# Kernel tuning notes

Hardware: AMD Instinct MI355X
Metric: run time of the kernel (lower is better)

## Reference

```python
import jax, jax.numpy as jnp
import numpy as np

NUM_V, NUM_R, ARITY = 100000, 1000, 3
D, I, H = 128, 64, 128
B, N = 4096, 64


def setup_inputs() -> dict:
    key = jax.random.key(0)
    ks = jax.random.split(key, 11)
    return {
        "r": jax.random.randint(ks[0], (B, N), 0, NUM_R),
        "e": jax.random.randint(ks[1], (ARITY, B, N), 0, NUM_V),
        "V": jax.random.normal(ks[2], (NUM_V, D + I), dtype=jnp.float32),
        "R": jax.random.normal(ks[3], (NUM_R, D), dtype=jnp.float32),
        "P": jax.random.normal(ks[4], (ARITY, D), dtype=jnp.float32),
        "WV": jax.random.normal(ks[5], (D + I, H), dtype=jnp.float32) * (1.0 / np.sqrt(D + I)),
        "bV": jax.random.normal(ks[6], (H,), dtype=jnp.float32) * 0.01,
        "WR": jax.random.normal(ks[7], (D, H), dtype=jnp.float32) * (1.0 / np.sqrt(D)),
        "bR": jax.random.normal(ks[8], (H,), dtype=jnp.float32) * 0.01,
        "WP": jax.random.normal(ks[9], (D, H), dtype=jnp.float32) * (1.0 / np.sqrt(D)),
        "bP": jax.random.normal(ks[10], (H,), dtype=jnp.float32) * 0.01,
    }


def reference(r, e, V, R, P, WV, bV, WR, bR, WP, bP):
    # x = Rl(R[r]) : gather relation embeddings then project -> [B, N, H]
    x = jnp.einsum("bnd,dh->bnh", R[r], WR) + bR
    # Pl(P[i]) for all arity positions at once -> [A, H]
    pe = P @ WP + bP
    # Vl(V[e[i]]) for all positions: gather then project -> [A, B, N, H]
    ve = jnp.einsum("abnd,dh->abnh", V[e], WV) + bV
    # loop body x = x * Pl(P[i]) * Vl(V[e[i]]) == product over arity axis
    x = x * jnp.prod(pe[:, None, None, :] * ve, axis=0)
    # dropout is identity (p=0 / eval); reduce over neighbor axis
    return jnp.sum(x, axis=1)  # [B, H]
```

## Files before the change

### kernel.cpp

```cpp
#include <hip/hip_runtime.h>

#define NUM_V 100000
#define NUM_R 1000
#define ARITY 3
#define DD 128
#define DI 192
#define HH 128
#define BB 4096
#define NN 64

typedef __attribute__((ext_vector_type(4))) float f32x4;
typedef __attribute__((ext_vector_type(8))) _Float16 half8;
typedef __attribute__((ext_vector_type(2))) _Float16 half2v;

__device__ inline void gload16(const void* g, void* lds) {
    __builtin_amdgcn_global_load_lds(
        (const __attribute__((address_space(1))) unsigned int*)g,
        (__attribute__((address_space(3))) unsigned int*)lds, 16, 0, 0);
}

__global__ __launch_bounds__(256) void prep_kernel(
    const float* __restrict__ R, const float* __restrict__ WR, const float* __restrict__ bR,
    _Float16* __restrict__ RWh,
    const float* __restrict__ WV, unsigned short* __restrict__ wf,
    const float* __restrict__ P, const float* __restrict__ WP, const float* __restrict__ bP,
    float* __restrict__ peProd) {
    const int bid = blockIdx.x;
    const int tid = threadIdx.x;

    if (bid < 32) {
        const int lane = tid & 63;
        const int wave = tid >> 6;
        const int wavesPerGrid = 32 * 4;
        const int waveId = bid * 4 + wave;
        const float2 b2 = ((const float2*)bR)[lane];
        const float2* __restrict__ W2 = (const float2*)WR;
        for (int rowBase0 = waveId * 8; rowBase0 < NUM_R; rowBase0 += wavesPerGrid * 8) {
            const int rowBase = __builtin_amdgcn_readfirstlane(rowBase0);
            float2 acc[8];
#pragma unroll
            for (int r8 = 0; r8 < 8; ++r8) acc[r8] = make_float2(0.f, 0.f);
#pragma unroll 4
            for (int k4 = 0; k4 < DD / 4; ++k4) {
                float4 v[8];
#pragma unroll
                for (int r8 = 0; r8 < 8; ++r8)
                    v[r8] = ((const float4*)(R + (size_t)(rowBase + r8) * DD))[k4];
#pragma unroll
                for (int kk = 0; kk < 4; ++kk) {
                    float2 w = W2[(k4 * 4 + kk) * 64 + lane];
#pragma unroll
                    for (int r8 = 0; r8 < 8; ++r8) {
                        float vv = (kk == 0) ? v[r8].x : (kk == 1) ? v[r8].y : (kk == 2) ? v[r8].z : v[r8].w;
                        acc[r8].x += vv * w.x;
                        acc[r8].y += vv * w.y;
                    }
                }
            }
#pragma unroll
            for (int r8 = 0; r8 < 8; ++r8) {
                if (rowBase + r8 < NUM_R) {
                    half2v h;
                    h.x = (_Float16)(acc[r8].x + b2.x);
                    h.y = (_Float16)(acc[r8].y + b2.y);
                    *(half2v*)(RWh + (size_t)(rowBase + r8) * HH + lane * 2) = h;
                }
            }
        }
    } else if (bid < 80) {
        if (tid < 64) {
            const int wb = bid - 32;
            const int ks = wb >> 3;
            const int ct = wb & 7;
            const int l = tid;
            const int col = ct * 16 + (l & 15);
            const int k0 = ks * 32 + (l >> 4) * 8;
            size_t base = (size_t)(ks * 8 + ct) * 512;
#pragma unroll
            for (int j = 0; j < 8; ++j) {
                float v = WV[(size_t)(k0 + j) * HH + col];
                wf[base + l * 8 + j] = __builtin_bit_cast(unsigned short, (_Float16)v);
            }
        }
    } else {
        if (tid < HH) {
            int h = tid;
            float prod = 1.0f;
            for (int a = 0; a < ARITY; ++a) {
                float acc = bP[h];
                for (int d = 0; d < DD; ++d) acc += P[a * DD + d] * WP[d * HH + h];
                prod *= acc;
            }
            peProd[h] = prod;
        }
    }
}

__global__ __launch_bounds__(832) void gemm_bres(const float* __restrict__ A,
                                                 const unsigned short* __restrict__ wf,
                                                 const float* __restrict__ bias,
                                                 _Float16* __restrict__ C, int M) {
    __shared__ unsigned short bsm[24576];
    __shared__ float aslots[13][2][1024];

    const int tid = threadIdx.x;
    const int l = tid & 63;
    const int wv = tid >> 6;

    const int tile = wv * 256 + blockIdx.x;
    const int rowbase = tile * 32;
    const bool active = rowbase < M;

    float bcol[8];
#pragma unroll
    for (int ct = 0; ct < 8; ++ct) bcol[ct] = bias[ct * 16 + (l & 15)];

    const float* aSrc = A + (size_t)(rowbase + (l >> 3)) * DI + (((l & 7) ^ (l >> 3)) << 2);

    int aoff[2][2];
#pragma unroll
    for (int rt = 0; rt < 2; ++rt) {
        const int Rr = rt * 16 + (l & 15);
        const int q = l >> 4;
#pragma unroll
        for (int k = 0; k < 2; ++k)
            aoff[rt][k] = Rr * 32 + (((2 * q + k) ^ (Rr & 7)) << 2);
    }

    f32x4 acc[2][8];
#pragma unroll
    for (int rt = 0; rt < 2; ++rt)
#pragma unroll
        for (int ct = 0; ct < 8; ++ct) acc[rt][ct] = (f32x4){0.f, 0.f, 0.f, 0.f};

#define STAGE_A(slot, ks)                                                   \
    do {                                                                    \
        _Pragma("unroll") for (int i = 0; i < 4; ++i)                       \
            gload16(aSrc + (ks) * 32 + i * 8 * DI, &aslots[wv][slot][i * 256]); \
    } while (0)

#define WAITV(n) asm volatile("s_waitcnt vmcnt(" #n ")" ::: "memory")

    if (active) {
        STAGE_A(0, 0);
        STAGE_A(1, 1);
    }
    if (wv < 12) {
#pragma unroll
        for (int i = 0; i < 4; ++i) {
            const int off = wv * 4096 + i * 1024;
            gload16((const char*)wf + off + l * 16, (char*)bsm + off);
        }
    }

    __syncthreads();
    if (!active) return;

#pragma unroll
    for (int ks = 0; ks < 6; ++ks) {
        const int slot = ks & 1;

        if (ks == 2 || ks == 3 || ks == 4) {
            WAITV(4);
            __builtin_amdgcn_sched_barrier(0);
        } else if (ks == 5) {
            WAITV(0);
            __builtin_amdgcn_sched_barrier(0);
        }

        f32x4 av[2][2];
#pragma unroll
        for (int rt = 0; rt < 2; ++rt) {
            av[rt][0] = *(const f32x4*)&aslots[wv][slot][aoff[rt][0]];
            av[rt][1] = *(const f32x4*)&aslots[wv][slot][aoff[rt][1]];
        }
        half8 bh[8];
#pragma unroll
        for (int ct = 0; ct < 8; ++ct)
            bh[ct] = *(const half8*)&bsm[(ks * 8 + ct) * 512 + l * 8];

        asm volatile("s_waitcnt lgkmcnt(0)" ::: "memory");
        __builtin_amdgcn_sched_barrier(0);

        if (ks < 4) STAGE_A(slot, ks + 2);

        half8 ah[2];
#pragma unroll
        for (int rt = 0; rt < 2; ++rt) {
            half8 t;
            t[0] = (_Float16)av[rt][0].x;
            t[1] = (_Float16)av[rt][0].y;
            t[2] = (_Float16)av[rt][0].z;
            t[3] = (_Float16)av[rt][0].w;
            t[4] = (_Float16)av[rt][1].x;
            t[5] = (_Float16)av[rt][1].y;
            t[6] = (_Float16)av[rt][1].z;
            t[7] = (_Float16)av[rt][1].w;
            ah[rt] = t;
        }

#pragma unroll
        for (int ct = 0; ct < 8; ++ct) {
#pragma unroll
            for (int rt = 0; rt < 2; ++rt)
                acc[rt][ct] = __builtin_amdgcn_mfma_f32_16x16x32_f16(ah[rt], bh[ct], acc[rt][ct], 0, 0, 0);
        }
    }
#undef STAGE_A
#undef WAITV

#pragma unroll
    for (int rt = 0; rt < 2; ++rt) {
        const int rb = rowbase + rt * 16 + (l >> 4) * 4;
#pragma unroll
        for (int j = 0; j < 4; ++j) {
            const int row = rb + j;
            if (row < M) {
#pragma unroll
                for (int ct = 0; ct < 8; ++ct)
                    C[(size_t)row * HH + ct * 16 + (l & 15)] = (_Float16)(acc[rt][ct][j] + bcol[ct]);
            }
        }
    }
}

__global__ __launch_bounds__(256) void gather_kernel(const int* __restrict__ r,
                                                     const int* __restrict__ e,
                                                     const _Float16* __restrict__ VWh,
                                                     const _Float16* __restrict__ RWh,
                                                     const float* __restrict__ peProd,
                                                     float* __restrict__ out) {
    __shared__ int rIdx[NN];
    __shared__ int eIdx[ARITY][NN];
    __shared__ float4 partial[3][16][2];

    const int b = blockIdx.x;
    const int tid = threadIdx.x;

    if (tid < NN) {
        rIdx[tid] = r[b * NN + tid];
    } else {
        int t = tid - NN;
        eIdx[t >> 6][t & 63] = e[(size_t)(t >> 6) * BB * NN + b * NN + (t & 63)];
    }
    __syncthreads();

    const int lane = tid & 63;
    const int wv = tid >> 6;
    const int q = lane >> 4;
    const int ho = lane & 15;

    float acc8[8];
#pragma unroll
    for (int k = 0; k < 8; ++k) acc8[k] = 0.f;

#pragma unroll
    for (int it = 0; it < 4; ++it) {
        int n = it * 16 + wv * 4 + q;
        half8 rw = *(const half8*)(RWh + (size_t)rIdx[n] * HH + ho * 8);
        half8 v0 = *(const half8*)(VWh + (size_t)eIdx[0][n] * HH + ho * 8);
        half8 v1 = *(const half8*)(VWh + (size_t)eIdx[1][n] * HH + ho * 8);
        half8 v2 = *(const half8*)(VWh + (size_t)eIdx[2][n] * HH + ho * 8);
        half8 p = rw * v0;
        p = p * v1;
        p = p * v2;
#pragma unroll
        for (int k = 0; k < 8; ++k) acc8[k] += (float)p[k];
    }

#pragma unroll
    for (int k = 0; k < 8; ++k) {
        acc8[k] += __shfl_xor(acc8[k], 16);
        acc8[k] += __shfl_xor(acc8[k], 32);
    }

    if (wv > 0 && lane < 16) {
        partial[wv - 1][ho][0] = make_float4(acc8[0], acc8[1], acc8[2], acc8[3]);
        partial[wv - 1][ho][1] = make_float4(acc8[4], acc8[5], acc8[6], acc8[7]);
    }
    __syncthreads();
    if (wv == 0 && lane < 16) {
        float4 s0 = make_float4(acc8[0], acc8[1], acc8[2], acc8[3]);
        float4 s1 = make_float4(acc8[4], acc8[5], acc8[6], acc8[7]);
#pragma unroll
        for (int g = 0; g < 3; ++g) {
            float4 t0 = partial[g][ho][0], t1 = partial[g][ho][1];
            s0.x += t0.x; s0.y += t0.y; s0.z += t0.z; s0.w += t0.w;
            s1.x += t1.x; s1.y += t1.y; s1.z += t1.z; s1.w += t1.w;
        }
        float4 p0 = ((const float4*)peProd)[ho * 2];
        float4 p1 = ((const float4*)peProd)[ho * 2 + 1];
        ((float4*)(out + (size_t)b * HH))[ho * 2] =
            make_float4(s0.x * p0.x, s0.y * p0.y, s0.z * p0.z, s0.w * p0.w);
        ((float4*)(out + (size_t)b * HH))[ho * 2 + 1] =
            make_float4(s1.x * p1.x, s1.y * p1.y, s1.z * p1.z, s1.w * p1.w);
    }
}

extern "C" void kernel_launch(void* const* d_in, const int* in_sizes, int n_in,
                              void* d_out, int out_size, void* d_ws, size_t ws_size,
                              hipStream_t stream) {
    const int* r = (const int*)d_in[0];
    const int* e = (const int*)d_in[1];
    const float* V = (const float*)d_in[2];
    const float* R = (const float*)d_in[3];
    const float* P = (const float*)d_in[4];
    const float* WV = (const float*)d_in[5];
    const float* bV = (const float*)d_in[6];
    const float* WR = (const float*)d_in[7];
    const float* bR = (const float*)d_in[8];
    const float* WP = (const float*)d_in[9];
    const float* bP = (const float*)d_in[10];
    float* out = (float*)d_out;

    _Float16* VWh = (_Float16*)d_ws;
    _Float16* RWh = VWh + (size_t)NUM_V * HH;
    float* peProd = (float*)(RWh + (size_t)NUM_R * HH);
    unsigned short* wfrag = (unsigned short*)(peProd + HH);

    prep_kernel<<<81, 256, 0, stream>>>(R, WR, bR, RWh, WV, wfrag, P, WP, bP, peProd);
    gemm_bres<<<256, 832, 0, stream>>>(V, wfrag, bV, VWh, NUM_V);
    gather_kernel<<<BB, 256, 0, stream>>>(r, e, VWh, RWh, peProd, out);
}
```

Measured before the change: 70.46 us.

## Replace 13-wave GEMM with 6-wave persistent multi-tile kernel loading B from global

Measured after the change: 87.78 us. +24.6%, slower.

```diff
diff --git a/kernel.cpp b/kernel.cpp
--- a/kernel.cpp
+++ b/kernel.cpp
@@ -96,129 +96,118 @@
     }
 }
 
-__global__ __launch_bounds__(832) void gemm_bres(const float* __restrict__ A,
-                                                 const unsigned short* __restrict__ wf,
-                                                 const float* __restrict__ bias,
-                                                 _Float16* __restrict__ C, int M) {
-    __shared__ unsigned short bsm[24576];
-    __shared__ float aslots[13][2][1024];
+__global__ __launch_bounds__(384) void gemm_dense(const float* __restrict__ A,
+                                                  const unsigned short* __restrict__ wf,
+                                                  const float* __restrict__ bias,
+                                                  _Float16* __restrict__ C, int M) {
+    __shared__ float atile[6][32 * DI];
 
     const int tid = threadIdx.x;
     const int l = tid & 63;
     const int wv = tid >> 6;
 
-    const int tile = wv * 256 + blockIdx.x;
-    const int rowbase = tile * 32;
-    const bool active = rowbase < M;
+    const int slot = blockIdx.x + 256 * wv;
+    const int ntile = (slot < 53) ? 3 : 2;
 
     float bcol[8];
 #pragma unroll
     for (int ct = 0; ct < 8; ++ct) bcol[ct] = bias[ct * 16 + (l & 15)];
 
-    const float* aSrc = A + (size_t)(rowbase + (l >> 3)) * DI + (((l & 7) ^ (l >> 3)) << 2);
-
-    int aoff[2][2];
+    int srcoff[24];
+#pragma unroll
+    for (int i = 0; i < 24; ++i) {
+        const int p = i * 64 + l;
+        const int r = p / 48;
+        const int cp = p - r * 48;
+        srcoff[i] = r * DI + ((cp ^ (r & 7)) << 2);
+    }
+
+    int aoffb[2][2];
 #pragma unroll
     for (int rt = 0; rt < 2; ++rt) {
         const int Rr = rt * 16 + (l & 15);
         const int q = l >> 4;
 #pragma unroll
         for (int k = 0; k < 2; ++k)
-            aoff[rt][k] = Rr * 32 + (((2 * q + k) ^ (Rr & 7)) << 2);
-    }
-
-    f32x4 acc[2][8];
-#pragma unroll
-    for (int rt = 0; rt < 2; ++rt)
-#pragma unroll
-        for (int ct = 0; ct < 8; ++ct) acc[rt][ct] = (f32x4){0.f, 0.f, 0.f, 0.f};
-
-#define STAGE_A(slot, ks)                                                   \
-    do {                                                                    \
-        _Pragma("unroll") for (int i = 0; i < 4; ++i)                       \
-            gload16(aSrc + (ks) * 32 + i * 8 * DI, &aslots[wv][slot][i * 256]); \
-    } while (0)
-
-#define WAITV(n) asm volatile("s_waitcnt vmcnt(" #n ")" ::: "memory")
-
-    if (active) {
-        STAGE_A(0, 0);
-        STAGE_A(1, 1);
-    }
-    if (wv < 12) {
-#pragma unroll
-        for (int i = 0; i < 4; ++i) {
-            const int off = wv * 4096 + i * 1024;
-            gload16((const char*)wf + off + l * 16, (char*)bsm + off);
-        }
-    }
-
-    __syncthreads();
-    if (!active) return;
-
-#pragma unroll
-    for (int ks = 0; ks < 6; ++ks) {
-        const int slot = ks & 1;
-
-        if (ks == 2 || ks == 3 || ks == 4) {
-            WAITV(4);
-            __builtin_amdgcn_sched_barrier(0);
-        } else if (ks == 5) {
-            WAITV(0);
-            __builtin_amdgcn_sched_barrier(0);
-        }
-
-        f32x4 av[2][2];
-#pragma unroll
-        for (int rt = 0; rt < 2; ++rt) {
-            av[rt][0] = *(const f32x4*)&aslots[wv][slot][aoff[rt][0]];
-            av[rt][1] = *(const f32x4*)&aslots[wv][slot][aoff[rt][1]];
-        }
-        half8 bh[8];
-#pragma unroll
-        for (int ct = 0; ct < 8; ++ct)
-            bh[ct] = *(const half8*)&bsm[(ks * 8 + ct) * 512 + l * 8];
+            aoffb[rt][k] = Rr * DI + (((2 * q + k) ^ (Rr & 7)) << 2);
+    }
+
+    const unsigned short* Bb = wf + l * 8;
+
+    for (int t = 0; t < ntile; ++t) {
+        const int tile = slot + t * 1536;
+        const int rowbase = tile * 32;
+        const float* Aw = A + (size_t)rowbase * DI;
 
         asm volatile("s_waitcnt lgkmcnt(0)" ::: "memory");
         __builtin_amdgcn_sched_barrier(0);
 
-        if (ks < 4) STAGE_A(slot, ks + 2);
-
-        half8 ah[2];
+#pragma unroll
+        for (int i = 0; i < 24; ++i)
+            gload16(Aw + srcoff[i], (char*)&atile[wv][0] + i * 1024);
+        __builtin_amdgcn_sched_barrier(0);
+
+        half8 bh[2][8];
+#pragma unroll
+        for (int ct = 0; ct < 8; ++ct)
+            bh[0][ct] = *(const half8*)(Bb + (size_t)(0 * 8 + ct) * 512);
+        __builtin_amdgcn_sched_barrier(0);
+
+        asm volatile("s_waitcnt vmcnt(8)" ::: "memory");
+        __builtin_amdgcn_sched_barrier(0);
+
+        f32x4 acc[2][8];
+#pragma unroll
+        for (int rt = 0; rt < 2; ++rt)
+#pragma unroll
+            for (int ct = 0; ct < 8; ++ct) acc[rt][ct] = (f32x4){0.f, 0.f, 0.f, 0.f};
+
+#pragma unroll
+        for (int ks = 0; ks < 6; ++ks) {
+            f32x4 av[2][2];
+#pragma unroll
+            for (int rt = 0; rt < 2; ++rt) {
+                av[rt][0] = *(const f32x4*)&atile[wv][aoffb[rt][0] + ks * 32];
+                av[rt][1] = *(const f32x4*)&atile[wv][aoffb[rt][1] + ks * 32];
+            }
+            if (ks < 5) {
+#pragma unroll
+                for (int ct = 0; ct < 8; ++ct)
+                    bh[(ks + 1) & 1][ct] = *(const half8*)(Bb + (size_t)((ks + 1) * 8 + ct) * 512);
+            }
+            half8 ah[2];
+#pragma unroll
+            for (int rt = 0; rt < 2; ++rt) {
+                half8 tt;
+                tt[0] = (_Float16)av[rt][0].x;
+                tt[1] = (_Float16)av[rt][0].y;
+                tt[2] = (_Float16)av[rt][0].z;
+                tt[3] = (_Float16)av[rt][0].w;
+                tt[4] = (_Float16)av[rt][1].x;
+                tt[5] = (_Float16)av[rt][1].y;
+                tt[6] = (_Float16)av[rt][1].z;
+                tt[7] = (_Float16)av[rt][1].w;
+                ah[rt] = tt;
+            }
+#pragma unroll
+            for (int ct = 0; ct < 8; ++ct) {
+#pragma unroll
+                for (int rt = 0; rt < 2; ++rt)
+                    acc[rt][ct] = __builtin_amdgcn_mfma_f32_16x16x32_f16(ah[rt], bh[ks & 1][ct], acc[rt][ct], 0, 0, 0);
+            }
+        }
+
 #pragma unroll
         for (int rt = 0; rt < 2; ++rt) {
-            half8 t;
-            t[0] = (_Float16)av[rt][0].x;
-            t[1] = (_Float16)av[rt][0].y;
-            t[2] = (_Float16)av[rt][0].z;
-            t[3] = (_Float16)av[rt][0].w;
-            t[4] = (_Float16)av[rt][1].x;
-            t[5] = (_Float16)av[rt][1].y;
-            t[6] = (_Float16)av[rt][1].z;
-            t[7] = (_Float16)av[rt][1].w;
-            ah[rt] = t;
-        }
-
-#pragma unroll
-        for (int ct = 0; ct < 8; ++ct) {
-#pragma unroll
-            for (int rt = 0; rt < 2; ++rt)
-                acc[rt][ct] = __builtin_amdgcn_mfma_f32_16x16x32_f16(ah[rt], bh[ct], acc[rt][ct], 0, 0, 0);
-        }
-    }
-#undef STAGE_A
-#undef WAITV
-
-#pragma unroll
-    for (int rt = 0; rt < 2; ++rt) {
-        const int rb = rowbase + rt * 16 + (l >> 4) * 4;
-#pragma unroll
-        for (int j = 0; j < 4; ++j) {
-            const int row = rb + j;
-            if (row < M) {
-#pragma unroll
-                for (int ct = 0; ct < 8; ++ct)
-                    C[(size_t)row * HH + ct * 16 + (l & 15)] = (_Float16)(acc[rt][ct][j] + bcol[ct]);
+            const int rb = rowbase + rt * 16 + (l >> 4) * 4;
+#pragma unroll
+            for (int j = 0; j < 4; ++j) {
+                const int row = rb + j;
+                if (row < M) {
+#pragma unroll
+                    for (int ct = 0; ct < 8; ++ct)
+                        C[(size_t)row * HH + ct * 16 + (l & 15)] = (_Float16)(acc[rt][ct][j] + bcol[ct]);
+                }
             }
         }
     }
@@ -319,6 +308,6 @@
     unsigned short* wfrag = (unsigned short*)(peProd + HH);
 
     prep_kernel<<<81, 256, 0, stream>>>(R, WR, bR, RWh, WV, wfrag, P, WP, bP, peProd);
-    gemm_bres<<<256, 832, 0, stream>>>(V, wfrag, bV, VWh, NUM_V);
+    gemm_dense<<<256, 384, 0, stream>>>(V, wfrag, bV, VWh, NUM_V);
     gather_kernel<<<BB, 256, 0, stream>>>(r, e, VWh, RWh, peProd, out);
 }
```
